# Optimization experiments

Hardware: AMD Instinct MI355X
Metric: run time of the kernel (lower is better)

Reference implementation:

```python
import jax, jax.numpy as jnp
import numpy as np


def setup_inputs() -> dict:
    key = jax.random.key(0)
    k1, k2 = jax.random.split(key)
    B, L, D = 8, 2048, 256
    x = jax.random.normal(k1, (B, L, D), dtype=jnp.float32)
    x_mask = jax.random.randint(k2, (B, L), 0, 2).astype(bool)  # True = padded key position
    return {"x": x, "x_mask": x_mask}


def reference(x, x_mask):
    # x: [B, L, D], x_mask: [B, L] bool (True = masked/padding)
    B, L, D = x.shape
    # Unscaled self-attention scores: [B, L, L]
    scores = jnp.einsum('bld,bmd->blm', x, x)
    # Diagonal exclusion: score of token with itself set to 0 (not -inf!)
    eye = jnp.eye(L, dtype=bool)
    scores = jnp.where(eye[None, :, :], jnp.float32(0.0), scores)
    # Padding mask: mask key columns with -inf (applied after diagonal zeroing,
    # so a masked diagonal entry ends up -inf, matching the torch order of ops)
    scores = jnp.where(x_mask[:, None, :], -jnp.inf, scores)
    a = jax.nn.softmax(scores, axis=2)
    return jnp.einsum('blm,bmd->bld', a, x)
```

## Files before the change

kernel.cpp:

```cpp
#include <hip/hip_runtime.h>
#include <hip/hip_bf16.h>

#define B_ 8
#define L_ 2048
#define D_ 256
#define BK 32
#define KSPLIT 2
#define KQ (L_/KSPLIT)
#define NIT (KQ/BK)
#define PSTR 40
#define NROW (B_*L_)
#define NE ((size_t)B_*L_*D_)

typedef __attribute__((ext_vector_type(8))) _Float16 f16x8;
typedef __attribute__((ext_vector_type(4))) _Float16 hf4;
typedef __attribute__((ext_vector_type(4))) float f32x4;

#define MFMA16F(a,b,c) __builtin_amdgcn_mfma_f32_16x16x32_f16((a),(b),(c),0,0,0)
#define NEG_INF (-__builtin_inff())
#define GLL(src,dst) __builtin_amdgcn_global_load_lds( \
    (const __attribute__((address_space(1))) void*)(src), \
    (__attribute__((address_space(3))) void*)(dst), 16, 0, 0)

__device__ __forceinline__ f32x4 fmax4(f32x4 a, f32x4 b){
  f32x4 r;
  r[0]=fmaxf(a[0],b[0]); r[1]=fmaxf(a[1],b[1]);
  r[2]=fmaxf(a[2],b[2]); r[3]=fmaxf(a[3],b[3]);
  return r;
}

__global__ void prep_k(const float* __restrict__ x,
                       _Float16* __restrict__ x16,
                       _Float16* __restrict__ vtl){
  __shared__ _Float16 T[64][258];
  const int t = threadIdx.x;
  const int l0 = blockIdx.x*64, b = blockIdx.y;
  const int r = t>>5, c = (t&31)*8;
  #pragma unroll
  for (int p=0;p<8;++p){
    int row = r + p*8;
    size_t idx = ((size_t)(b*L_ + l0 + row))*D_ + c;
    float4 v0 = *(const float4*)(x + idx);
    float4 v1 = *(const float4*)(x + idx + 4);
    f16x8 h;
    h[0]=(_Float16)v0.x; h[1]=(_Float16)v0.y; h[2]=(_Float16)v0.z; h[3]=(_Float16)v0.w;
    h[4]=(_Float16)v1.x; h[5]=(_Float16)v1.y; h[6]=(_Float16)v1.z; h[7]=(_Float16)v1.w;
    *(f16x8*)(x16 + idx) = h;
    #pragma unroll
    for (int j=0;j<8;++j) T[row][c+j] = h[j];
  }
  __syncthreads();
  _Float16* vb = vtl + ((size_t)(b*64 + blockIdx.x*2))*8192;
  #pragma unroll
  for (int i=0;i<8;++i){
    int n = t + 256*i;
    int q = n & 1023, tile = n>>10;
    int d = q>>2, ph = q&3;
    int kc = ph ^ ((d>>1)&3);
    int k0 = tile*32 + kc*8;
    f16x8 h;
    #pragma unroll
    for (int j=0;j<8;++j) h[j] = T[k0+j][d];
    *(f16x8*)(vb + (size_t)n*8) = h;
  }
}

__launch_bounds__(256, 2)
__global__ void rowmax_k(const _Float16* __restrict__ x16,
                         const int* __restrict__ mask,
                         float* __restrict__ pmax){
  __shared__ __attribute__((aligned(16))) _Float16 sK[2][8192];

  const int tid  = threadIdx.x;
  const int wave = tid >> 6, lane = tid & 63;
  const int quad = lane >> 4, l16 = lane & 15;
  const int b = blockIdx.y, z = blockIdx.z;
  const int q0w = blockIdx.x*64 + wave*16;
  const int sw = l16 & 7;

  f16x8 qh[8];
  {
    const _Float16* qr = x16 + ((size_t)(b*L_ + q0w + l16))*D_;
    #pragma unroll
    for (int ks=0; ks<8; ++ks)
      qh[ks] = *(const f16x8*)(qr + ks*32 + quad*8);
  }
  unsigned long long mb = 0;
  {
    const int* mrow = mask + b*L_ + z*KQ;
    #pragma unroll
    for (int j=0;j<64;++j)
      mb |= (unsigned long long)(mrow[j*16 + l16] ? 1u : 0u) << j;
  }

  unsigned kof[4], dof[4];
  #pragma unroll
  for (int i=0;i<4;++i){
    int c = (wave + i*4)*64 + lane;
    int r = c>>5, pk = c&31;
    kof[i] = (unsigned)(r*512 + ((pk ^ (r&7))*16));
    dof[i] = (unsigned)((wave + i*4)*1024);
  }
  const char* kbase = (const char*)x16 + ((size_t)b*L_ + (size_t)z*KQ)*(D_*2);
  #pragma unroll
  for (int i=0;i<4;++i) GLL(kbase + kof[i], (char*)sK[0] + dof[i]);

  f32x4 macc = (f32x4){NEG_INF,NEG_INF,NEG_INF,NEG_INF};
  __syncthreads();

  for (int it=0; it<NIT; ++it){
    if (it+1 < NIT){
      const char* kb2 = kbase + (size_t)(it+1)*16384;
      char* kd = (char*)sK[(it+1)&1];
      #pragma unroll
      for (int i=0;i<4;++i) GLL(kb2 + kof[i], kd + dof[i]);
    }
    const _Float16* kb = sK[it&1];

    f32x4 S[2];
    S[0]=(f32x4){0,0,0,0}; S[1]=(f32x4){0,0,0,0};
    #pragma unroll
    for (int ks=0; ks<8; ++ks){
      f16x8 b0 = *(const f16x8*)(kb + (     l16)*256 + (((ks*4+quad)^sw)*8));
      f16x8 b1 = *(const f16x8*)(kb + (16 + l16)*256 + (((ks*4+quad)^sw)*8));
      S[0] = MFMA16F(qh[ks], b0, S[0]);
      S[1] = MFMA16F(qh[ks], b1, S[1]);
    }
    {
      const int d0 = q0w - (z*KQ + it*BK);
      if ((unsigned)d0 < 32u){
        const int ntd = d0 >> 4;
        #pragma unroll
        for (int r=0;r<4;++r)
          S[ntd][r] = (l16 == quad*4+r) ? 0.0f : S[ntd][r];
      }
    }
    {
      const unsigned mw = (unsigned)(mb >> (unsigned)(it*2));
      const float mk0 = (mw & 1u) ? NEG_INF : 0.0f;
      const float mk1 = (mw & 2u) ? NEG_INF : 0.0f;
      #pragma unroll
      for (int r=0;r<4;++r){ S[0][r] += mk0; S[1][r] += mk1; }
    }
    macc = fmax4(macc, fmax4(S[0], S[1]));

    __syncthreads();
  }

  f32x4 t = macc;
  #pragma unroll
  for (int off=1; off<16; off<<=1){
    f32x4 o;
    o[0]=__shfl_xor(t[0],off); o[1]=__shfl_xor(t[1],off);
    o[2]=__shfl_xor(t[2],off); o[3]=__shfl_xor(t[3],off);
    t = fmax4(t,o);
  }
  if (l16 == 0){
    const int row = b*L_ + q0w + quad*4;
    #pragma unroll
    for (int r=0;r<4;++r) pmax[z*NROW + row + r] = t[r];
  }
}

__launch_bounds__(256, 2)
__global__ void flash_k(const _Float16* __restrict__ x16,
                        const _Float16* __restrict__ vtl,
                        const int* __restrict__ mask,
                        const float* __restrict__ pmax,
                        _Float16* __restrict__ oall,
                        float* __restrict__ mll){
  __shared__ __attribute__((aligned(16))) _Float16 sK[2][8192];
  __shared__ __attribute__((aligned(16))) _Float16 sV[2][8192];
  __shared__ __attribute__((aligned(16))) _Float16 sP[4][16*PSTR];

  const int tid  = threadIdx.x;
  const int wave = tid >> 6, lane = tid & 63;
  const int quad = lane >> 4, l16 = lane & 15;
  const int b = blockIdx.y, z = blockIdx.z;
  const int q0w = blockIdx.x*64 + wave*16;
  const int sw = l16 & 7, vsw = (l16>>1)&3;

  f16x8 qh[8];
  {
    const _Float16* qr = x16 + ((size_t)(b*L_ + q0w + l16))*D_;
    #pragma unroll
    for (int ks=0; ks<8; ++ks)
      qh[ks] = *(const f16x8*)(qr + ks*32 + quad*8);
  }
  unsigned long long mb = 0;
  {
    const int* mrow = mask + b*L_ + z*KQ;
    #pragma unroll
    for (int j=0;j<64;++j)
      mb |= (unsigned long long)(mrow[j*16 + l16] ? 1u : 0u) << j;
  }

  f32x4 M;
  {
    const int row0 = b*L_ + q0w + quad*4;
    M = fmax4(*(const f32x4*)(pmax + row0),
              *(const f32x4*)(pmax + NROW + row0));
  }

  unsigned kof[4], vof[4], dof[4];
  #pragma unroll
  for (int i=0;i<4;++i){
    int c = (wave + i*4)*64 + lane;
    int r = c>>5, pk = c&31;
    kof[i] = (unsigned)(r*512 + ((pk ^ (r&7))*16));
    vof[i] = (unsigned)(c*16);
    dof[i] = (unsigned)((wave + i*4)*1024);
  }
  const char* kbase = (const char*)x16 + ((size_t)b*L_ + (size_t)z*KQ)*(D_*2);
  const char* vbase = (const char*)vtl + ((size_t)(b*64 + z*32))*16384;

  #pragma unroll
  for (int i=0;i<4;++i){
    GLL(kbase + kof[i], (char*)sK[0] + dof[i]);
    GLL(vbase + vof[i], (char*)sV[0] + dof[i]);
  }

  f32x4 O[16], Osum;
  #pragma unroll
  for (int i=0;i<16;i++) O[i] = (f32x4){0.f,0.f,0.f,0.f};
  Osum = (f32x4){0.f,0.f,0.f,0.f};
  f16x8 ones;
  #pragma unroll
  for (int j=0;j<8;++j) ones[j] = (_Float16)1.0f;

  __syncthreads();

  for (int it=0; it<NIT; ++it){
    if (it+1 < NIT){
      const char* kb2 = kbase + (size_t)(it+1)*16384;
      const char* vb2 = vbase + (size_t)(it+1)*16384;
      char* kd = (char*)sK[(it+1)&1];
      char* vd = (char*)sV[(it+1)&1];
      #pragma unroll
      for (int i=0;i<4;++i){
        GLL(kb2 + kof[i], kd + dof[i]);
        GLL(vb2 + vof[i], vd + dof[i]);
      }
    }
    const _Float16* kb = sK[it&1];
    const _Float16* vb = sV[it&1];

    f32x4 S[2];
    S[0]=(f32x4){0,0,0,0}; S[1]=(f32x4){0,0,0,0};
    #pragma unroll
    for (int ks=0; ks<8; ++ks){
      f16x8 b0 = *(const f16x8*)(kb + (     l16)*256 + (((ks*4+quad)^sw)*8));
      f16x8 b1 = *(const f16x8*)(kb + (16 + l16)*256 + (((ks*4+quad)^sw)*8));
      S[0] = MFMA16F(qh[ks], b0, S[0]);
      S[1] = MFMA16F(qh[ks], b1, S[1]);
    }

    {
      const int d0 = q0w - (z*KQ + it*BK);
      if ((unsigned)d0 < 32u){
        const int ntd = d0 >> 4;
        #pragma unroll
        for (int r=0;r<4;++r)
          S[ntd][r] = (l16 == quad*4+r) ? 0.0f : S[ntd][r];
      }
    }
    {
      const unsigned mw = (unsigned)(mb >> (unsigned)(it*2));
      const float mk0 = (mw & 1u) ? NEG_INF : 0.0f;
      const float mk1 = (mw & 2u) ? NEG_INF : 0.0f;
      #pragma unroll
      for (int r=0;r<4;++r){ S[0][r] += mk0; S[1][r] += mk1; }
    }

    #pragma unroll
    for (int r=0;r<4;++r){
      const int row = quad*4 + r;
      sP[wave][row*PSTR +      l16] = (_Float16)__expf(S[0][r] - M[r]);
      sP[wave][row*PSTR + 16 + l16] = (_Float16)__expf(S[1][r] - M[r]);
    }
    __threadfence_block();
    f16x8 pf = *(const f16x8*)(&sP[wave][l16*PSTR + quad*8]);

    #pragma unroll
    for (int vt=0; vt<16; ++vt){
      f16x8 bv = *(const f16x8*)(vb + (vt*16+l16)*32 + ((quad^vsw)*8));
      O[vt] = MFMA16F(pf, bv, O[vt]);
    }
    Osum = MFMA16F(pf, ones, Osum);

    __syncthreads();
  }

  {
    const int u = b*(L_/16) + blockIdx.x*4 + wave;
    _Float16* ob = oall + (size_t)z*NE + (size_t)u*4096;
    #pragma unroll
    for (int vt=0; vt<16; ++vt){
      hf4 hh;
      #pragma unroll
      for (int r=0;r<4;++r) hh[r] = (_Float16)O[vt][r];
      *(hf4*)(ob + vt*256 + lane*4) = hh;
    }
    if (l16 == 0){
      const int row = u*16 + quad*4;
      #pragma unroll
      for (int r=0;r<4;++r) mll[z*NROW + row + r] = Osum[r];
    }
  }
}

__global__ void combine_k(float* __restrict__ out,
                          const _Float16* __restrict__ oall,
                          const float* __restrict__ mll){
  __shared__ float T2[16][260];
  const int t = threadIdx.x, u = blockIdx.x;
  const int quad = (t>>4)&3, l16 = t&15;
  const int row0 = u*16 + quad*4;

  f32x4 den = (f32x4){0.f,0.f,0.f,0.f};
  #pragma unroll
  for (int zc=0; zc<KSPLIT; ++zc)
    den += *(const f32x4*)(mll + zc*NROW + row0);
  float inv[4];
  #pragma unroll
  for (int r=0;r<4;++r) inv[r] = 1.0f/den[r];

  #pragma unroll
  for (int i=0;i<4;++i){
    const int f = t + 256*i;
    const int vt = f>>6;
    float acc[4] = {0.f,0.f,0.f,0.f};
    #pragma unroll
    for (int zc=0; zc<KSPLIT; ++zc){
      hf4 v = *(const hf4*)(oall + (size_t)zc*NE + (size_t)u*4096 + (size_t)f*4);
      #pragma unroll
      for (int r=0;r<4;++r) acc[r] += (float)v[r];
    }
    #pragma unroll
    for (int r=0;r<4;++r) T2[quad*4+r][vt*16+l16] = acc[r]*inv[r];
  }
  __syncthreads();
  #pragma unroll
  for (int p=0;p<4;++p){
    const int row = (t>>6) + p*4, col = (t&63)*4;
    float4 vv = *(const float4*)&T2[row][col];
    *(float4*)(out + ((size_t)u*16 + row)*D_ + col) = vv;
  }
}

extern "C" void kernel_launch(void* const* d_in, const int* in_sizes, int n_in,
                              void* d_out, int out_size, void* d_ws, size_t ws_size,
                              hipStream_t stream) {
  const float* x    = (const float*)d_in[0];
  const int*   mask = (const int*)d_in[1];
  float*       out  = (float*)d_out;

  _Float16* x16  = (_Float16*)d_ws;
  _Float16* vtl  = x16 + NE;
  _Float16* oall = vtl + NE;
  float*    mll  = (float*)(oall + (size_t)KSPLIT*NE);
  float*    pmax = mll + (size_t)KSPLIT*NROW;

  prep_k   <<<dim3(L_/64, B_), dim3(256), 0, stream>>>(x, x16, vtl);
  rowmax_k <<<dim3(L_/64, B_, KSPLIT), dim3(256), 0, stream>>>(x16, mask, pmax);
  flash_k  <<<dim3(L_/64, B_, KSPLIT), dim3(256), 0, stream>>>(x16, vtl, mask, pmax, oall, mll);
  combine_k<<<dim3(NROW/16), dim3(256), 0, stream>>>(out, oall, mll);
}
```

Before: 158.4 us.

## Replace separate row-max pass with lazy online softmax rescaling in flash kernel

Drops the rowmax kernel that recomputed the full QK^T product just to find exact row maxima. The flash kernel now keeps a running max per row and rescales the accumulators only when a wave sees a score more than a threshold above the current max. The combine kernel merges the split-K partial results using the per-split maxima. This removes roughly half of the QK matmul work, at the cost of a warp-vote branch per tile, occasional rescale passes, and fp16 accumulator values that may grow up to e^6 above the stored max.

```diff
diff --git a/kernel.cpp b/kernel.cpp
--- a/kernel.cpp
+++ b/kernel.cpp
@@ -11,6 +11,8 @@
 #define PSTR 40
 #define NROW (B_*L_)
 #define NE ((size_t)B_*L_*D_)
+#define THR 6.0f
+#define MINIT (-1e30f)
 
 typedef __attribute__((ext_vector_type(8))) _Float16 f16x8;
 typedef __attribute__((ext_vector_type(4))) _Float16 hf4;
@@ -66,109 +68,12 @@
 }
 
 __launch_bounds__(256, 2)
-__global__ void rowmax_k(const _Float16* __restrict__ x16,
-                         const int* __restrict__ mask,
-                         float* __restrict__ pmax){
-  __shared__ __attribute__((aligned(16))) _Float16 sK[2][8192];
-
-  const int tid  = threadIdx.x;
-  const int wave = tid >> 6, lane = tid & 63;
-  const int quad = lane >> 4, l16 = lane & 15;
-  const int b = blockIdx.y, z = blockIdx.z;
-  const int q0w = blockIdx.x*64 + wave*16;
-  const int sw = l16 & 7;
-
-  f16x8 qh[8];
-  {
-    const _Float16* qr = x16 + ((size_t)(b*L_ + q0w + l16))*D_;
-    #pragma unroll
-    for (int ks=0; ks<8; ++ks)
-      qh[ks] = *(const f16x8*)(qr + ks*32 + quad*8);
-  }
-  unsigned long long mb = 0;
-  {
-    const int* mrow = mask + b*L_ + z*KQ;
-    #pragma unroll
-    for (int j=0;j<64;++j)
-      mb |= (unsigned long long)(mrow[j*16 + l16] ? 1u : 0u) << j;
-  }
-
-  unsigned kof[4], dof[4];
-  #pragma unroll
-  for (int i=0;i<4;++i){
-    int c = (wave + i*4)*64 + lane;
-    int r = c>>5, pk = c&31;
-    kof[i] = (unsigned)(r*512 + ((pk ^ (r&7))*16));
-    dof[i] = (unsigned)((wave + i*4)*1024);
-  }
-  const char* kbase = (const char*)x16 + ((size_t)b*L_ + (size_t)z*KQ)*(D_*2);
-  #pragma unroll
-  for (int i=0;i<4;++i) GLL(kbase + kof[i], (char*)sK[0] + dof[i]);
-
-  f32x4 macc = (f32x4){NEG_INF,NEG_INF,NEG_INF,NEG_INF};
-  __syncthreads();
-
-  for (int it=0; it<NIT; ++it){
-    if (it+1 < NIT){
-      const char* kb2 = kbase + (size_t)(it+1)*16384;
-      char* kd = (char*)sK[(it+1)&1];
-      #pragma unroll
-      for (int i=0;i<4;++i) GLL(kb2 + kof[i], kd + dof[i]);
-    }
-    const _Float16* kb = sK[it&1];
-
-    f32x4 S[2];
-    S[0]=(f32x4){0,0,0,0}; S[1]=(f32x4){0,0,0,0};
-    #pragma unroll
-    for (int ks=0; ks<8; ++ks){
-      f16x8 b0 = *(const f16x8*)(kb + (     l16)*256 + (((ks*4+quad)^sw)*8));
-      f16x8 b1 = *(const f16x8*)(kb + (16 + l16)*256 + (((ks*4+quad)^sw)*8));
-      S[0] = MFMA16F(qh[ks], b0, S[0]);
-      S[1] = MFMA16F(qh[ks], b1, S[1]);
-    }
-    {
-      const int d0 = q0w - (z*KQ + it*BK);
-      if ((unsigned)d0 < 32u){
-        const int ntd = d0 >> 4;
-        #pragma unroll
-        for (int r=0;r<4;++r)
-          S[ntd][r] = (l16 == quad*4+r) ? 0.0f : S[ntd][r];
-      }
-    }
-    {
-      const unsigned mw = (unsigned)(mb >> (unsigned)(it*2));
-      const float mk0 = (mw & 1u) ? NEG_INF : 0.0f;
-      const float mk1 = (mw & 2u) ? NEG_INF : 0.0f;
-      #pragma unroll
-      for (int r=0;r<4;++r){ S[0][r] += mk0; S[1][r] += mk1; }
-    }
-    macc = fmax4(macc, fmax4(S[0], S[1]));
-
-    __syncthreads();
-  }
-
-  f32x4 t = macc;
-  #pragma unroll
-  for (int off=1; off<16; off<<=1){
-    f32x4 o;
-    o[0]=__shfl_xor(t[0],off); o[1]=__shfl_xor(t[1],off);
-    o[2]=__shfl_xor(t[2],off); o[3]=__shfl_xor(t[3],off);
-    t = fmax4(t,o);
-  }
-  if (l16 == 0){
-    const int row = b*L_ + q0w + quad*4;
-    #pragma unroll
-    for (int r=0;r<4;++r) pmax[z*NROW + row + r] = t[r];
-  }
-}
-
-__launch_bounds__(256, 2)
 __global__ void flash_k(const _Float16* __restrict__ x16,
                         const _Float16* __restrict__ vtl,
                         const int* __restrict__ mask,
-                        const float* __restrict__ pmax,
                         _Float16* __restrict__ oall,
-                        float* __restrict__ mll){
+                        float* __restrict__ mll,
+                        float* __restrict__ mm){
   __shared__ __attribute__((aligned(16))) _Float16 sK[2][8192];
   __shared__ __attribute__((aligned(16))) _Float16 sV[2][8192];
   __shared__ __attribute__((aligned(16))) _Float16 sP[4][16*PSTR];
@@ -195,12 +100,7 @@
       mb |= (unsigned long long)(mrow[j*16 + l16] ? 1u : 0u) << j;
   }
 
-  f32x4 M;
-  {
-    const int row0 = b*L_ + q0w + quad*4;
-    M = fmax4(*(const f32x4*)(pmax + row0),
-              *(const f32x4*)(pmax + NROW + row0));
-  }
+  f32x4 M = (f32x4){MINIT, MINIT, MINIT, MINIT};
 
   unsigned kof[4], vof[4], dof[4];
   #pragma unroll
@@ -272,6 +172,37 @@
       for (int r=0;r<4;++r){ S[0][r] += mk0; S[1][r] += mk1; }
     }
 
+    {
+      int ok = 1;
+      #pragma unroll
+      for (int r=0;r<4;++r){
+        ok &= (S[0][r] <= M[r] + THR);
+        ok &= (S[1][r] <= M[r] + THR);
+      }
+      if (!__all(ok)){
+        f32x4 t = fmax4(S[0], S[1]);
+        #pragma unroll
+        for (int off=1; off<16; off<<=1){
+          f32x4 o;
+          o[0]=__shfl_xor(t[0],off); o[1]=__shfl_xor(t[1],off);
+          o[2]=__shfl_xor(t[2],off); o[3]=__shfl_xor(t[3],off);
+          t = fmax4(t,o);
+        }
+        f32x4 mn = fmax4(M, t);
+        float sc[4];
+        #pragma unroll
+        for (int r=0;r<4;++r) sc[r] = __expf(M[r] - mn[r]);
+        #pragma unroll
+        for (int vt=0; vt<16; ++vt){
+          #pragma unroll
+          for (int r=0;r<4;++r) O[vt][r] *= sc[r];
+        }
+        #pragma unroll
+        for (int r=0;r<4;++r) Osum[r] *= sc[r];
+        M = mn;
+      }
+    }
+
     #pragma unroll
     for (int r=0;r<4;++r){
       const int row = quad*4 + r;
@@ -304,23 +235,43 @@
     if (l16 == 0){
       const int row = u*16 + quad*4;
       #pragma unroll
-      for (int r=0;r<4;++r) mll[z*NROW + row + r] = Osum[r];
+      for (int r=0;r<4;++r){
+        mll[z*NROW + row + r] = Osum[r];
+        mm [z*NROW + row + r] = M[r];
+      }
     }
   }
 }
 
 __global__ void combine_k(float* __restrict__ out,
                           const _Float16* __restrict__ oall,
-                          const float* __restrict__ mll){
+                          const float* __restrict__ mll,
+                          const float* __restrict__ mm){
   __shared__ float T2[16][260];
   const int t = threadIdx.x, u = blockIdx.x;
   const int quad = (t>>4)&3, l16 = t&15;
   const int row0 = u*16 + quad*4;
 
+  f32x4 mz[KSPLIT], lz[KSPLIT];
+  #pragma unroll
+  for (int zc=0; zc<KSPLIT; ++zc){
+    mz[zc] = *(const f32x4*)(mm  + zc*NROW + row0);
+    lz[zc] = *(const f32x4*)(mll + zc*NROW + row0);
+  }
+  f32x4 ms = mz[0];
+  #pragma unroll
+  for (int zc=1; zc<KSPLIT; ++zc) ms = fmax4(ms, mz[zc]);
+
+  float sc[KSPLIT][4];
   f32x4 den = (f32x4){0.f,0.f,0.f,0.f};
   #pragma unroll
-  for (int zc=0; zc<KSPLIT; ++zc)
-    den += *(const f32x4*)(mll + zc*NROW + row0);
+  for (int zc=0; zc<KSPLIT; ++zc){
+    #pragma unroll
+    for (int r=0;r<4;++r){
+      sc[zc][r] = __expf(mz[zc][r] - ms[r]);
+      den[r] += sc[zc][r] * lz[zc][r];
+    }
+  }
   float inv[4];
   #pragma unroll
   for (int r=0;r<4;++r) inv[r] = 1.0f/den[r];
@@ -334,7 +285,7 @@
     for (int zc=0; zc<KSPLIT; ++zc){
       hf4 v = *(const hf4*)(oall + (size_t)zc*NE + (size_t)u*4096 + (size_t)f*4);
       #pragma unroll
-      for (int r=0;r<4;++r) acc[r] += (float)v[r];
+      for (int r=0;r<4;++r) acc[r] += sc[zc][r] * (float)v[r];
     }
     #pragma unroll
     for (int r=0;r<4;++r) T2[quad*4+r][vt*16+l16] = acc[r]*inv[r];
@@ -359,10 +310,9 @@
   _Float16* vtl  = x16 + NE;
   _Float16* oall = vtl + NE;
   float*    mll  = (float*)(oall + (size_t)KSPLIT*NE);
-  float*    pmax = mll + (size_t)KSPLIT*NROW;
+  float*    mm   = mll + (size_t)KSPLIT*NROW;
 
   prep_k   <<<dim3(L_/64, B_), dim3(256), 0, stream>>>(x, x16, vtl);
-  rowmax_k <<<dim3(L_/64, B_, KSPLIT), dim3(256), 0, stream>>>(x16, mask, pmax);
-  flash_k  <<<dim3(L_/64, B_, KSPLIT), dim3(256), 0, stream>>>(x16, vtl, mask, pmax, oall, mll);
-  combine_k<<<dim3(NROW/16), dim3(256), 0, stream>>>(out, oall, mll);
-}
+  flash_k  <<<dim3(L_/64, B_, KSPLIT), dim3(256), 0, stream>>>(x16, vtl, mask, oall, mll, mm);
+  combine_k<<<dim3(NROW/16), dim3(256), 0, stream>>>(out, oall, mll, mm);
+}
```

Result: faster. 149.7 us (-5.5%).
